# Kernel tuning notes

Hardware: AMD Instinct MI355X
Metric: run time of the kernel (lower is better)

The kernel has to match this reference:

```python
import jax, jax.numpy as jnp
import numpy as np

N = 40000        # nodes (shared across categories)
E = 600000       # edges per category graph
H = 2            # heads
C = 64           # hidden (out_channels per head)
IN_DIMS = [128, 128, 64]
FUSED = H * C * len(IN_DIMS)  # 384


def setup_inputs() -> dict:
    key = jax.random.key(0)
    ks = iter(jax.random.split(key, 64))
    d = {}
    for i, din in enumerate(IN_DIMS):
        d[f"x{i}"] = jax.random.normal(next(ks), (N, din), jnp.float32)
        d[f"ei{i}"] = jax.random.randint(next(ks), (2, E), 0, N)
        d[f"W{i}"] = jax.random.normal(next(ks), (din, H * C), jnp.float32) / np.sqrt(din)
        d[f"att_s{i}"] = jax.random.normal(next(ks), (H, C), jnp.float32) * 0.1
        d[f"att_d{i}"] = jax.random.normal(next(ks), (H, C), jnp.float32) * 0.1
        d[f"bias{i}"] = jnp.zeros((H * C,), jnp.float32)
    d["Wc1"] = jax.random.normal(next(ks), (FUSED, 128), jnp.float32) / np.sqrt(FUSED)
    d["bc1"] = jnp.zeros((128,), jnp.float32)
    d["Wc2"] = jax.random.normal(next(ks), (128, 1), jnp.float32) / np.sqrt(128.0)
    d["bc2"] = jnp.zeros((1,), jnp.float32)
    return d


def gat_conv(x, edge_index, W, att_s, att_d, bias):
    """PyG GATConv (concat=True, add_self_loops=True, eval mode)."""
    n = x.shape[0]
    xw = (x @ W).reshape(n, H, C)                       # [N,H,C]
    a_src = jnp.einsum('nhc,hc->nh', xw, att_s)         # [N,H]
    a_dst = jnp.einsum('nhc,hc->nh', xw, att_d)         # [N,H]
    loop = jnp.arange(n)
    src = jnp.concatenate([edge_index[0], loop])        # [E+N]
    dst = jnp.concatenate([edge_index[1], loop])
    e = jax.nn.leaky_relu(a_src[src] + a_dst[dst], 0.2)  # [E+N,H]
    # segment softmax over incoming edges per destination node
    m = jax.lax.stop_gradient(jax.ops.segment_max(e, dst, num_segments=n))
    ex = jnp.exp(e - m[dst])
    s = jax.ops.segment_sum(ex, dst, num_segments=n)
    alpha = ex / s[dst]                                  # [E+N,H]
    out = jax.ops.segment_sum(xw[src] * alpha[..., None], dst, num_segments=n)
    return out.reshape(n, H * C) + bias


def reference(x0, ei0, W0, att_s0, att_d0, bias0,
              x1, ei1, W1, att_s1, att_d1, bias1,
              x2, ei2, W2, att_s2, att_d2, bias2,
              Wc1, bc1, Wc2, bc2):
    h0 = jax.nn.elu(gat_conv(x0, ei0, W0, att_s0, att_d0, bias0))
    h1 = jax.nn.elu(gat_conv(x1, ei1, W1, att_s1, att_d1, bias1))
    h2 = jax.nn.elu(gat_conv(x2, ei2, W2, att_s2, att_d2, bias2))
    Hcat = jnp.concatenate([h0, h1, h2], axis=-1)        # [N, FUSED]
    hid = jax.nn.relu(Hcat @ Wc1 + bc1)
    return hid @ Wc2 + bc2                               # [N, 1]
```

## Files before the change

kernel.cpp:

```cpp
#include <hip/hip_runtime.h>
#include <cstdint>
#include <cstddef>


__device__ __forceinline__ float lrelu02(float x) { return x > 0.f ? x : 0.2f * x; }
__device__ __forceinline__ float elu1(float x) { return x > 0.f ? x : (__expf(x) - 1.f); }

__device__ __forceinline__ unsigned bfrne(float x) {
  unsigned u = __float_as_uint(x);
  return (u + 0x7FFFu + ((u >> 16) & 1u)) >> 16;
}
__device__ __forceinline__ unsigned pack2bf(float lo, float hi) {
  return bfrne(lo) | (bfrne(hi) << 16);
}
__device__ __forceinline__ float bflo2f(unsigned u) { return __uint_as_float(u << 16); }
__device__ __forceinline__ float bfhi2f(unsigned u) { return __uint_as_float(u & 0xFFFF0000u); }

typedef __attribute__((ext_vector_type(8))) short short8;
typedef __attribute__((ext_vector_type(4))) float f32x4;

#define SLICES 8
#define CAPX 448
#define BCAP (SLICES * CAPX)

#define SBS 512
#define SEPT 16
#define STB (SBS * SEPT)
#define NBINS_PAD 1024

__global__ void zeroB(int* __restrict__ a, int n) {
  int i = blockIdx.x * blockDim.x + threadIdx.x;
  if (i < n) a[i] = 0;
}

__global__ void w_swz(const float* __restrict__ W,
                      unsigned short* __restrict__ wsw, int nt) {
  int idx = blockIdx.x * blockDim.x + threadIdx.x;
  if (idx >= nt * 8 * 64) return;
  int l = idx & 63;
  int n = (idx >> 6) & 7;
  int t = idx >> 9;
  int col = n * 16 + (l & 15);
  int kbase = t * 32 + (l >> 4) * 8;
  uint4 o;
  o.x = pack2bf(W[(kbase + 0) * 128 + col], W[(kbase + 1) * 128 + col]);
  o.y = pack2bf(W[(kbase + 2) * 128 + col], W[(kbase + 3) * 128 + col]);
  o.z = pack2bf(W[(kbase + 4) * 128 + col], W[(kbase + 5) * 128 + col]);
  o.w = pack2bf(W[(kbase + 6) * 128 + col], W[(kbase + 7) * 128 + col]);
  *(uint4*)(wsw + (size_t)idx * 8) = o;
}

__global__ __launch_bounds__(256) void gemm_att_mfma(
    const float* __restrict__ X, const unsigned short* __restrict__ wsw,
    const float* __restrict__ att_s, const float* __restrict__ att_d,
    unsigned short* __restrict__ XWH, float* __restrict__ a_src,
    float* __restrict__ a_dst, int M, int K) {
  const int tid = threadIdx.x;
  const int l = tid & 63;
  const int w = tid >> 6;
  const int lrow = l & 15;
  const int lk = (l >> 4) * 8;
  const int row0 = blockIdx.x * 64 + w * 16;
  int arow = row0 + lrow; if (arow >= M) arow = M - 1;
  const float* aptr = X + (size_t)arow * K + lk;
  const unsigned short* bptr = wsw + (size_t)l * 8;
  const int nt = K >> 5;

  f32x4 acc[8];
#pragma unroll
  for (int n = 0; n < 8; ++n) acc[n] = (f32x4){0.f, 0.f, 0.f, 0.f};

  for (int t = 0; t < nt; ++t) {
    float4 xa = *(const float4*)(aptr + t * 32);
    float4 xb = *(const float4*)(aptr + t * 32 + 4);
    uint4 av;
    av.x = pack2bf(xa.x, xa.y);
    av.y = pack2bf(xa.z, xa.w);
    av.z = pack2bf(xb.x, xb.y);
    av.w = pack2bf(xb.z, xb.w);
    short8 af = __builtin_bit_cast(short8, av);
#pragma unroll
    for (int n = 0; n < 8; ++n) {
      uint4 bv = *(const uint4*)(bptr + (size_t)(t * 8 + n) * 512);
      short8 bf = __builtin_bit_cast(short8, bv);
      acc[n] = __builtin_amdgcn_mfma_f32_16x16x32_bf16(af, bf, acc[n], 0, 0, 0);
    }
  }

  float as_[8], ad_[8];
#pragma unroll
  for (int n = 0; n < 8; ++n) {
    int col = n * 16 + lrow;
    as_[n] = att_s[col];
    ad_[n] = att_d[col];
  }
#pragma unroll
  for (int r = 0; r < 4; ++r) {
    int wrow = row0 + (l >> 4) * 4 + r;
    const bool ok = wrow < M;
    float ps0 = 0.f, ps1 = 0.f, pd0 = 0.f, pd1 = 0.f;
#pragma unroll
    for (int n = 0; n < 8; ++n) {
      float v = acc[n][r];
      if (ok) XWH[(size_t)wrow * 128 + n * 16 + lrow] = (unsigned short)bfrne(v);
      if (n < 4) { ps0 = fmaf(v, as_[n], ps0); pd0 = fmaf(v, ad_[n], pd0); }
      else       { ps1 = fmaf(v, as_[n], ps1); pd1 = fmaf(v, ad_[n], pd1); }
    }
#pragma unroll
    for (int off = 1; off < 16; off <<= 1) {
      ps0 += __shfl_xor(ps0, off); ps1 += __shfl_xor(ps1, off);
      pd0 += __shfl_xor(pd0, off); pd1 += __shfl_xor(pd1, off);
    }
    if (lrow == 0 && ok) {
      ((float2*)a_src)[wrow] = make_float2(ps0, ps1);
      ((float2*)a_dst)[wrow] = make_float2(pd0, pd1);
    }
  }
}

__global__ __launch_bounds__(512) void scatter_p(
    const int* __restrict__ ei0, const int* __restrict__ ei1,
    const int* __restrict__ ei2, int E0, int E1, int E2,
    int nbpc, int* __restrict__ bktCnt, int* __restrict__ bkt) {
  __shared__ int hist[NBINS_PAD];
  __shared__ int binStart[NBINS_PAD];
  __shared__ int binResv[NBINS_PAD];
  __shared__ int fillB[NBINS_PAD];
  __shared__ int scanBuf[SBS];
  __shared__ int stage[STB];
  __shared__ int gdst[STB];
  const int tid = threadIdx.x;
  const int slice = blockIdx.x & (SLICES - 1);
  const int nbins = 3 * nbpc;
  const int c1 = E0, c2 = E0 + E1, totE = c2 + E2;
  const int eb = blockIdx.x * STB;

  for (int b = tid; b < NBINS_PAD; b += SBS) hist[b] = 0;
  __syncthreads();

  int binv[SEPT], payv[SEPT];
#pragma unroll
  for (int k = 0; k < SEPT; ++k) {
    int g = eb + k * SBS + tid;
    int bn = -1, pay = 0;
    if (g < totE) {
      int s, d, cat;
      if (g < c1)      { s = ei0[g]; d = ei0[E0 + g]; cat = 0; }
      else if (g < c2) { int t = g - c1; s = ei1[t]; d = ei1[E1 + t]; cat = 1; }
      else             { int t = g - c2; s = ei2[t]; d = ei2[E2 + t]; cat = 2; }
      bn = cat * nbpc + (d >> 7);
      pay = ((d & 127) << 16) | s;
      atomicAdd(&hist[bn], 1);
    }
    binv[k] = bn; payv[k] = pay;
  }
  __syncthreads();

  const int a0 = hist[tid * 2], a1 = hist[tid * 2 + 1];
  scanBuf[tid] = a0 + a1;
  __syncthreads();
  for (int off = 1; off < SBS; off <<= 1) {
    int v = (tid >= off) ? scanBuf[tid - off] : 0;
    __syncthreads();
    scanBuf[tid] += v;
    __syncthreads();
  }
  const int total = scanBuf[SBS - 1];
  const int base = (tid > 0) ? scanBuf[tid - 1] : 0;
  binStart[tid * 2] = base;
  binStart[tid * 2 + 1] = base + a0;

  for (int b = tid; b < NBINS_PAD; b += SBS) {
    fillB[b] = 0;
    int c = hist[b];
    if (c > 0 && b < nbins)
      binResv[b] = atomicAdd(&bktCnt[(b * SLICES + slice) * 16], c);
  }
  __syncthreads();

#pragma unroll
  for (int k = 0; k < SEPT; ++k) {
    int bn = binv[k];
    if (bn >= 0) {
      int f = atomicAdd(&fillB[bn], 1);
      int p = binStart[bn] + f;
      int go = binResv[bn] + f;
      stage[p] = payv[k];
      gdst[p] = (go < CAPX) ? ((bn * SLICES + slice) * CAPX + go) : -1;
    }
  }
  __syncthreads();

  for (int i = tid; i < total; i += SBS) {
    int g = gdst[i];
    if (g >= 0) bkt[g] = stage[i];
  }
}

__global__ __launch_bounds__(256) void sortbkt(
    int* __restrict__ bkt, const int* __restrict__ bktCnt,
    int2* __restrict__ offcnt, int Nn, int nbpc) {
  __shared__ int cntA[128], scanA[128], fillA[128];
  __shared__ int esort[BCAP];
  const int tid = threadIdx.x;
  const int b = blockIdx.x;
  const int cat = b / nbpc, bl = b - cat * nbpc, dBase = bl << 7;
  if (tid < 128) {
    cntA[tid] = (dBase + tid < Nn) ? 1 : 0;
    fillA[tid] = 0;
  }
  __syncthreads();
  int ns[SLICES];
#pragma unroll
  for (int s = 0; s < SLICES; ++s)
    ns[s] = min(bktCnt[(b * SLICES + s) * 16], CAPX);
#pragma unroll
  for (int s = 0; s < SLICES; ++s) {
    const int* seg = bkt + (size_t)(b * SLICES + s) * CAPX;
    for (int i = tid; i < ns[s]; i += 256) atomicAdd(&cntA[seg[i] >> 16], 1);
  }
  __syncthreads();
  if (tid < 128) scanA[tid] = cntA[tid];
  __syncthreads();
  for (int off = 1; off < 128; off <<= 1) {
    int t = (tid < 128 && tid >= off) ? scanA[tid - off] : 0;
    __syncthreads();
    if (tid < 128) scanA[tid] += t;
    __syncthreads();
  }
#pragma unroll
  for (int s = 0; s < SLICES; ++s) {
    const int* seg = bkt + (size_t)(b * SLICES + s) * CAPX;
    for (int i = tid; i < ns[s]; i += 256) {
      int v = seg[i];
      int n = v >> 16;
      int p = scanA[n] - cntA[n] + atomicAdd(&fillA[n], 1);
      esort[p] = v & 0xFFFF;
    }
  }
  if (tid < 128 && dBase + tid < Nn) esort[scanA[tid] - 1] = dBase + tid;
  __syncthreads();
  const int tot = scanA[127];
  int* outp = bkt + (size_t)b * BCAP;
  for (int i = tid; i < tot; i += 256) outp[i] = esort[i];
  if (tid < 128 && dBase + tid < Nn)
    offcnt[(size_t)cat * Nn + dBase + tid] =
        make_int2(b * BCAP + scanA[tid] - cntA[tid], cntA[tid]);
}

__global__ __launch_bounds__(256) void aggregate(
    const unsigned short* __restrict__ xwh, const float* __restrict__ a_src,
    const float* __restrict__ a_dst, const int2* __restrict__ offcnt,
    const int* __restrict__ adjS, const float* __restrict__ bias,
    unsigned short* __restrict__ ahc, int Nn) {
  const int node = (int)((blockIdx.x * (size_t)blockDim.x + threadIdx.x) >> 6);
  const int lane = threadIdx.x & 63;
  if (node >= Nn) return;
  const int2 oc = offcnt[node];
  const int base = oc.x, end = oc.x + oc.y;
  const float2 ad = ((const float2*)a_dst)[node];

  float m0 = -1e30f, s0 = 0.f, m1 = -1e30f, s1 = 0.f;
  int sv0 = 0; float ex0 = -1e30f, ey0 = -1e30f;
  for (int cb = base; cb < end; cb += 64) {
    int j = cb + lane;
    int sv = 0; float ex = -1e30f, ey = -1e30f;
    if (j < end) {
      sv = adjS[j];
      float2 as = ((const float2*)a_src)[sv];
      ex = lrelu02(as.x + ad.x);
      ey = lrelu02(as.y + ad.y);
      float nm0 = fmaxf(m0, ex);
      s0 = s0 * __expf(m0 - nm0) + __expf(ex - nm0); m0 = nm0;
      float nm1 = fmaxf(m1, ey);
      s1 = s1 * __expf(m1 - nm1) + __expf(ey - nm1); m1 = nm1;
    }
    if (cb == base) { sv0 = sv; ex0 = ex; ey0 = ey; }
  }
#pragma unroll
  for (int off = 32; off; off >>= 1) {
    float om0 = __shfl_xor(m0, off), os0 = __shfl_xor(s0, off);
    float nm0 = fmaxf(m0, om0);
    s0 = s0 * __expf(m0 - nm0) + os0 * __expf(om0 - nm0); m0 = nm0;
    float om1 = __shfl_xor(m1, off), os1 = __shfl_xor(s1, off);
    float nm1 = fmaxf(m1, om1);
    s1 = s1 * __expf(m1 - nm1) + os1 * __expf(om1 - nm1); m1 = nm1;
  }
  const float inv0 = 1.f / s0, inv1 = 1.f / s1;
  const bool h0 = (lane < 32);

  float2 acc = {0.f, 0.f};
  for (int cb = base; cb < end; cb += 64) {
    const int cnt = min(64, end - cb);
    int srcv; float w0v, w1v;
    if (cb == base) {
      srcv = sv0;
      w0v = __expf(ex0 - m0) * inv0;
      w1v = __expf(ey0 - m1) * inv1;
    } else {
      srcv = 0; float ex = -1e30f, ey = -1e30f;
      if (lane < cnt) {
        srcv = adjS[cb + lane];
        float2 as = ((const float2*)a_src)[srcv];
        ex = lrelu02(as.x + ad.x);
        ey = lrelu02(as.y + ad.y);
      }
      w0v = __expf(ex - m0) * inv0;
      w1v = __expf(ey - m1) * inv1;
    }
    int k = 0;
    for (; k + 4 <= cnt; k += 4) {
      int sa = __shfl(srcv, k),     sb = __shfl(srcv, k + 1);
      int sc = __shfl(srcv, k + 2), sd = __shfl(srcv, k + 3);
      unsigned ua = ((const unsigned*)(xwh + (size_t)sa * 128))[lane];
      unsigned ub = ((const unsigned*)(xwh + (size_t)sb * 128))[lane];
      unsigned uc = ((const unsigned*)(xwh + (size_t)sc * 128))[lane];
      unsigned ud = ((const unsigned*)(xwh + (size_t)sd * 128))[lane];
      float w0a = __shfl(w0v, k),     w1a = __shfl(w1v, k);
      float w0b = __shfl(w0v, k + 1), w1b = __shfl(w1v, k + 1);
      float w0c = __shfl(w0v, k + 2), w1c = __shfl(w1v, k + 2);
      float w0d = __shfl(w0v, k + 3), w1d = __shfl(w1v, k + 3);
      float wa = h0 ? w0a : w1a;
      float wb = h0 ? w0b : w1b;
      float wc = h0 ? w0c : w1c;
      float wd = h0 ? w0d : w1d;
      acc.x = fmaf(wa, bflo2f(ua), acc.x); acc.y = fmaf(wa, bfhi2f(ua), acc.y);
      acc.x = fmaf(wb, bflo2f(ub), acc.x); acc.y = fmaf(wb, bfhi2f(ub), acc.y);
      acc.x = fmaf(wc, bflo2f(uc), acc.x); acc.y = fmaf(wc, bfhi2f(uc), acc.y);
      acc.x = fmaf(wd, bflo2f(ud), acc.x); acc.y = fmaf(wd, bfhi2f(ud), acc.y);
    }
    for (; k < cnt; ++k) {
      int s = __shfl(srcv, k);
      float w0b_ = __shfl(w0v, k), w1b_ = __shfl(w1v, k);
      float w = h0 ? w0b_ : w1b_;
      unsigned u = ((const unsigned*)(xwh + (size_t)s * 128))[lane];
      acc.x = fmaf(w, bflo2f(u), acc.x);
      acc.y = fmaf(w, bfhi2f(u), acc.y);
    }
  }
  const float2 bv = ((const float2*)bias)[lane];
  ((unsigned*)(ahc + (size_t)node * 384))[lane] =
      pack2bf(elu1(acc.x + bv.x), elu1(acc.y + bv.y));
}

__global__ __launch_bounds__(256) void final_mlp_mfma(
    const unsigned short* __restrict__ ah, const unsigned short* __restrict__ wsw,
    const float* __restrict__ bc1, const float* __restrict__ Wc2,
    const float* __restrict__ bc2, float* __restrict__ out, int Nn) {
  const int tid = threadIdx.x;
  const int l = tid & 63;
  const int w = tid >> 6;
  const int lrow = l & 15;
  const int lk = (l >> 4) * 8;
  int row = blockIdx.x * 64 + w * 16 + lrow;
  int arow = row < Nn ? row : Nn - 1;
  const unsigned short* aptr = ah + (size_t)arow * 384 + lk;
  const unsigned short* bptr = wsw + (size_t)l * 8;

  f32x4 acc[8];
#pragma unroll
  for (int n = 0; n < 8; ++n) acc[n] = (f32x4){0.f, 0.f, 0.f, 0.f};

  for (int t = 0; t < 12; ++t) {
    uint4 av = *(const uint4*)(aptr + t * 32);
    short8 af = __builtin_bit_cast(short8, av);
#pragma unroll
    for (int n = 0; n < 8; ++n) {
      uint4 bv = *(const uint4*)(bptr + (size_t)(t * 8 + n) * 512);
      short8 bf = __builtin_bit_cast(short8, bv);
      acc[n] = __builtin_amdgcn_mfma_f32_16x16x32_bf16(af, bf, acc[n], 0, 0, 0);
    }
  }

  float bcv[8], w2v[8];
#pragma unroll
  for (int n = 0; n < 8; ++n) {
    int col = n * 16 + lrow;
    bcv[n] = bc1[col];
    w2v[n] = Wc2[col];
  }
  float p[4];
#pragma unroll
  for (int r = 0; r < 4; ++r) {
    float s = 0.f;
#pragma unroll
    for (int n = 0; n < 8; ++n)
      s = fmaf(fmaxf(acc[n][r] + bcv[n], 0.f), w2v[n], s);
#pragma unroll
    for (int off = 1; off < 16; off <<= 1) s += __shfl_xor(s, off);
    p[r] = s;
  }
  if (lrow == 0) {
    int orow = blockIdx.x * 64 + w * 16 + (l >> 4) * 4;
    float b2 = bc2[0];
    if (orow + 3 < Nn) {
      float4 o = {p[0] + b2, p[1] + b2, p[2] + b2, p[3] + b2};
      *(float4*)(out + orow) = o;
    } else {
#pragma unroll
      for (int r = 0; r < 4; ++r)
        if (orow + r < Nn) out[orow + r] = p[r] + b2;
    }
  }
}

extern "C" void kernel_launch(void* const* d_in, const int* in_sizes, int n_in,
                              void* d_out, int out_size, void* d_ws, size_t ws_size,
                              hipStream_t stream) {
  const int Nn = out_size;
  const int E0 = in_sizes[1] / 2;
  const int E1 = in_sizes[7] / 2;
  const int E2 = in_sizes[13] / 2;
  const int totE = E0 + E1 + E2;
  const int Nt = 3 * Nn;
  const int nbpc = (Nn + 127) / 128;
  const int NB = 3 * nbpc;

  char* base = (char*)d_ws;
  size_t off = 0;
  auto carve = [&](size_t bytes) -> void* {
    off = (off + 255) & ~(size_t)255;
    void* p = base + off;
    off += bytes;
    return p;
  };
  unsigned short* xwh = (unsigned short*)carve((size_t)Nn * 128 * 2);
  unsigned short* ah  = (unsigned short*)carve((size_t)Nn * 384 * 2);
  unsigned short* wsw = (unsigned short*)carve((size_t)12 * 8 * 64 * 8 * 2);
  unsigned short* wswx = (unsigned short*)carve((size_t)3 * 4 * 8 * 64 * 8 * 2);
  float* a_src3 = (float*)carve((size_t)Nt * 2 * 4);
  float* a_dst3 = (float*)carve((size_t)Nt * 2 * 4);
  int*  bktCnt  = (int*)carve((size_t)NB * SLICES * 16 * 4);
  int2* offcnt3 = (int2*)carve((size_t)Nt * 8);
  int*  bkt     = (int*)carve((size_t)NB * BCAP * 4);
  (void)ws_size; (void)n_in;

  const int* ei0 = (const int*)d_in[1];
  const int* ei1 = (const int*)d_in[7];
  const int* ei2 = (const int*)d_in[13];

  const int ncnt = NB * SLICES * 16;
  zeroB<<<(ncnt + 255) / 256, 256, 0, stream>>>(bktCnt, ncnt);
  w_swz<<<(12 * 8 * 64 + 255) / 256, 256, 0, stream>>>(
      (const float*)d_in[18], wsw, 12);
  for (int cat = 0; cat < 3; ++cat) {
    const int K = in_sizes[6 * cat] / Nn;
    w_swz<<<((K >> 5) * 8 * 64 + 255) / 256, 256, 0, stream>>>(
        (const float*)d_in[6 * cat + 2], wswx + (size_t)cat * 4 * 8 * 64 * 8,
        K >> 5);
  }
  scatter_p<<<(totE + STB - 1) / STB, SBS, 0, stream>>>(
      ei0, ei1, ei2, E0, E1, E2, nbpc, bktCnt, bkt);
  sortbkt<<<NB, 256, 0, stream>>>(bkt, bktCnt, offcnt3, Nn, nbpc);

  for (int cat = 0; cat < 3; ++cat) {
    const float* x   = (const float*)d_in[6 * cat + 0];
    const float* ats = (const float*)d_in[6 * cat + 3];
    const float* atd = (const float*)d_in[6 * cat + 4];
    const float* bia = (const float*)d_in[6 * cat + 5];
    const int K = in_sizes[6 * cat] / Nn;
    float* a_src_c = a_src3 + (size_t)cat * Nn * 2;
    float* a_dst_c = a_dst3 + (size_t)cat * Nn * 2;

    gemm_att_mfma<<<(Nn + 63) / 64, 256, 0, stream>>>(
        x, wswx + (size_t)cat * 4 * 8 * 64 * 8, ats, atd, xwh,
        a_src_c, a_dst_c, Nn, K);
    aggregate<<<((size_t)Nn * 64 + 255) / 256, 256, 0, stream>>>(
        xwh, a_src_c, a_dst_c, offcnt3 + (size_t)cat * Nn, bkt, bia,
        ah + (size_t)cat * 128, Nn);
  }

  final_mlp_mfma<<<(Nn + 63) / 64, 256, 0, stream>>>(
      ah, wsw, (const float*)d_in[19], (const float*)d_in[20],
      (const float*)d_in[21], (float*)d_out, Nn);
}
```

Before: 323.5 us.

## Aggregate four nodes per wavefront with 16-lane groups and 16-byte gathers

The GAT aggregation kernel now gives each destination node a 16-lane group instead of a full 64-lane wavefront, so one wave handles four nodes. Each lane loads 8 bf16 features with a uint4 gather and keeps 8 accumulators. Edge weights for both heads travel between lanes packed as fp16 pairs. This is meant to cut idle lanes for low-degree nodes (about 16 edges on average) and to issue fewer, wider memory transactions, at the cost of divergence across the four nodes, since the loop runs to the wave-wide maximum degree, and of fp16 rounding on the attention weights.

Result: faster. 296.6 us (-8.3%).

```diff
diff --git a/kernel.cpp b/kernel.cpp
--- a/kernel.cpp
+++ b/kernel.cpp
@@ -1,4 +1,5 @@
 #include <hip/hip_runtime.h>
+#include <hip/hip_fp16.h>
 #include <cstdint>
 #include <cstddef>
 
@@ -15,6 +16,17 @@
 }
 __device__ __forceinline__ float bflo2f(unsigned u) { return __uint_as_float(u << 16); }
 __device__ __forceinline__ float bfhi2f(unsigned u) { return __uint_as_float(u & 0xFFFF0000u); }
+
+__device__ __forceinline__ unsigned pack2half(float lo, float hi) {
+  __half2 h2 = __floats2half2_rn(lo, hi);
+  return __builtin_bit_cast(unsigned, h2);
+}
+__device__ __forceinline__ float h2lo(unsigned u) {
+  return __half2float(__low2half(__builtin_bit_cast(__half2, u)));
+}
+__device__ __forceinline__ float h2hi(unsigned u) {
+  return __half2float(__high2half(__builtin_bit_cast(__half2, u)));
+}
 
 typedef __attribute__((ext_vector_type(8))) short short8;
 typedef __attribute__((ext_vector_type(4))) float f32x4;
@@ -253,20 +265,25 @@
     const float* __restrict__ a_dst, const int2* __restrict__ offcnt,
     const int* __restrict__ adjS, const float* __restrict__ bias,
     unsigned short* __restrict__ ahc, int Nn) {
-  const int node = (int)((blockIdx.x * (size_t)blockDim.x + threadIdx.x) >> 6);
-  const int lane = threadIdx.x & 63;
-  if (node >= Nn) return;
-  const int2 oc = offcnt[node];
-  const int base = oc.x, end = oc.x + oc.y;
-  const float2 ad = ((const float2*)a_dst)[node];
+  const int tid = threadIdx.x;
+  const int lane = tid & 63;
+  const int li = lane & 15;
+  const int gb = lane & 48;
+  const int wid = (int)((blockIdx.x * (size_t)blockDim.x + tid) >> 6);
+  const int node = wid * 4 + (lane >> 4);
+  const bool nok = node < Nn;
+  const int cnode = nok ? node : Nn - 1;
+  const int2 oc = offcnt[cnode];
+  const int base = oc.x;
+  const int cnt = oc.y;
+  const float2 ad = ((const float2*)a_dst)[cnode];
 
   float m0 = -1e30f, s0 = 0.f, m1 = -1e30f, s1 = 0.f;
   int sv0 = 0; float ex0 = -1e30f, ey0 = -1e30f;
-  for (int cb = base; cb < end; cb += 64) {
-    int j = cb + lane;
+  for (int cb = 0; cb < cnt; cb += 16) {
     int sv = 0; float ex = -1e30f, ey = -1e30f;
-    if (j < end) {
-      sv = adjS[j];
+    if (cb + li < cnt) {
+      sv = adjS[base + cb + li];
       float2 as = ((const float2*)a_src)[sv];
       ex = lrelu02(as.x + ad.x);
       ey = lrelu02(as.y + ad.y);
@@ -275,10 +292,10 @@
       float nm1 = fmaxf(m1, ey);
       s1 = s1 * __expf(m1 - nm1) + __expf(ey - nm1); m1 = nm1;
     }
-    if (cb == base) { sv0 = sv; ex0 = ex; ey0 = ey; }
-  }
-#pragma unroll
-  for (int off = 32; off; off >>= 1) {
+    if (cb == 0) { sv0 = sv; ex0 = ex; ey0 = ey; }
+  }
+#pragma unroll
+  for (int off = 8; off; off >>= 1) {
     float om0 = __shfl_xor(m0, off), os0 = __shfl_xor(s0, off);
     float nm0 = fmaxf(m0, om0);
     s0 = s0 * __expf(m0 - nm0) + os0 * __expf(om0 - nm0); m0 = nm0;
@@ -287,60 +304,77 @@
     s1 = s1 * __expf(m1 - nm1) + os1 * __expf(om1 - nm1); m1 = nm1;
   }
   const float inv0 = 1.f / s0, inv1 = 1.f / s1;
-  const bool h0 = (lane < 32);
-
-  float2 acc = {0.f, 0.f};
-  for (int cb = base; cb < end; cb += 64) {
-    const int cnt = min(64, end - cb);
-    int srcv; float w0v, w1v;
-    if (cb == base) {
-      srcv = sv0;
-      w0v = __expf(ex0 - m0) * inv0;
-      w1v = __expf(ey0 - m1) * inv1;
-    } else {
-      srcv = 0; float ex = -1e30f, ey = -1e30f;
-      if (lane < cnt) {
-        srcv = adjS[cb + lane];
-        float2 as = ((const float2*)a_src)[srcv];
+
+  int mc = cnt;
+  mc = max(mc, __shfl_xor(mc, 16));
+  mc = max(mc, __shfl_xor(mc, 32));
+
+  const bool hlo = (li < 8);
+  float acc[8];
+#pragma unroll
+  for (int c = 0; c < 8; ++c) acc[c] = 0.f;
+
+  for (int cb = 0; cb < mc; cb += 16) {
+    int sv; float ex, ey;
+    if (cb == 0) { sv = sv0; ex = ex0; ey = ey0; }
+    else {
+      sv = 0; ex = -1e30f; ey = -1e30f;
+      if (cb + li < cnt) {
+        sv = adjS[base + cb + li];
+        float2 as = ((const float2*)a_src)[sv];
         ex = lrelu02(as.x + ad.x);
         ey = lrelu02(as.y + ad.y);
       }
-      w0v = __expf(ex - m0) * inv0;
-      w1v = __expf(ey - m1) * inv1;
-    }
+    }
+    const float w0 = __expf(ex - m0) * inv0;
+    const float w1 = __expf(ey - m1) * inv1;
+    const unsigned wpk = pack2half(w0, w1);
+
+    int cc = cnt - cb; cc = cc < 0 ? 0 : (cc > 16 ? 16 : cc);
+    cc = max(cc, __shfl_xor(cc, 16));
+    cc = max(cc, __shfl_xor(cc, 32));
+
     int k = 0;
-    for (; k + 4 <= cnt; k += 4) {
-      int sa = __shfl(srcv, k),     sb = __shfl(srcv, k + 1);
-      int sc = __shfl(srcv, k + 2), sd = __shfl(srcv, k + 3);
-      unsigned ua = ((const unsigned*)(xwh + (size_t)sa * 128))[lane];
-      unsigned ub = ((const unsigned*)(xwh + (size_t)sb * 128))[lane];
-      unsigned uc = ((const unsigned*)(xwh + (size_t)sc * 128))[lane];
-      unsigned ud = ((const unsigned*)(xwh + (size_t)sd * 128))[lane];
-      float w0a = __shfl(w0v, k),     w1a = __shfl(w1v, k);
-      float w0b = __shfl(w0v, k + 1), w1b = __shfl(w1v, k + 1);
-      float w0c = __shfl(w0v, k + 2), w1c = __shfl(w1v, k + 2);
-      float w0d = __shfl(w0v, k + 3), w1d = __shfl(w1v, k + 3);
-      float wa = h0 ? w0a : w1a;
-      float wb = h0 ? w0b : w1b;
-      float wc = h0 ? w0c : w1c;
-      float wd = h0 ? w0d : w1d;
-      acc.x = fmaf(wa, bflo2f(ua), acc.x); acc.y = fmaf(wa, bfhi2f(ua), acc.y);
-      acc.x = fmaf(wb, bflo2f(ub), acc.x); acc.y = fmaf(wb, bfhi2f(ub), acc.y);
-      acc.x = fmaf(wc, bflo2f(uc), acc.x); acc.y = fmaf(wc, bfhi2f(uc), acc.y);
-      acc.x = fmaf(wd, bflo2f(ud), acc.x); acc.y = fmaf(wd, bfhi2f(ud), acc.y);
-    }
-    for (; k < cnt; ++k) {
-      int s = __shfl(srcv, k);
-      float w0b_ = __shfl(w0v, k), w1b_ = __shfl(w1v, k);
-      float w = h0 ? w0b_ : w1b_;
-      unsigned u = ((const unsigned*)(xwh + (size_t)s * 128))[lane];
-      acc.x = fmaf(w, bflo2f(u), acc.x);
-      acc.y = fmaf(w, bfhi2f(u), acc.y);
-    }
-  }
-  const float2 bv = ((const float2*)bias)[lane];
-  ((unsigned*)(ahc + (size_t)node * 384))[lane] =
-      pack2bf(elu1(acc.x + bv.x), elu1(acc.y + bv.y));
+    for (; k + 2 <= cc; k += 2) {
+      int ska = __shfl(sv, gb + k);
+      int skb = __shfl(sv, gb + k + 1);
+      unsigned wka = __shfl(wpk, gb + k);
+      unsigned wkb = __shfl(wpk, gb + k + 1);
+      uint4 ua = *(const uint4*)(xwh + (size_t)ska * 128 + li * 8);
+      uint4 ub = *(const uint4*)(xwh + (size_t)skb * 128 + li * 8);
+      float wa = hlo ? h2lo(wka) : h2hi(wka);
+      float wb = hlo ? h2lo(wkb) : h2hi(wkb);
+      acc[0] = fmaf(wa, bflo2f(ua.x), acc[0]); acc[1] = fmaf(wa, bfhi2f(ua.x), acc[1]);
+      acc[2] = fmaf(wa, bflo2f(ua.y), acc[2]); acc[3] = fmaf(wa, bfhi2f(ua.y), acc[3]);
+      acc[4] = fmaf(wa, bflo2f(ua.z), acc[4]); acc[5] = fmaf(wa, bfhi2f(ua.z), acc[5]);
+      acc[6] = fmaf(wa, bflo2f(ua.w), acc[6]); acc[7] = fmaf(wa, bfhi2f(ua.w), acc[7]);
+      acc[0] = fmaf(wb, bflo2f(ub.x), acc[0]); acc[1] = fmaf(wb, bfhi2f(ub.x), acc[1]);
+      acc[2] = fmaf(wb, bflo2f(ub.y), acc[2]); acc[3] = fmaf(wb, bfhi2f(ub.y), acc[3]);
+      acc[4] = fmaf(wb, bflo2f(ub.z), acc[4]); acc[5] = fmaf(wb, bfhi2f(ub.z), acc[5]);
+      acc[6] = fmaf(wb, bflo2f(ub.w), acc[6]); acc[7] = fmaf(wb, bfhi2f(ub.w), acc[7]);
+    }
+    for (; k < cc; ++k) {
+      int sk = __shfl(sv, gb + k);
+      unsigned wk = __shfl(wpk, gb + k);
+      float w = hlo ? h2lo(wk) : h2hi(wk);
+      uint4 u = *(const uint4*)(xwh + (size_t)sk * 128 + li * 8);
+      acc[0] = fmaf(w, bflo2f(u.x), acc[0]); acc[1] = fmaf(w, bfhi2f(u.x), acc[1]);
+      acc[2] = fmaf(w, bflo2f(u.y), acc[2]); acc[3] = fmaf(w, bfhi2f(u.y), acc[3]);
+      acc[4] = fmaf(w, bflo2f(u.z), acc[4]); acc[5] = fmaf(w, bfhi2f(u.z), acc[5]);
+      acc[6] = fmaf(w, bflo2f(u.w), acc[6]); acc[7] = fmaf(w, bfhi2f(u.w), acc[7]);
+    }
+  }
+
+  if (nok) {
+    const float4 b0 = *(const float4*)(bias + li * 8);
+    const float4 b1 = *(const float4*)(bias + li * 8 + 4);
+    uint4 o;
+    o.x = pack2bf(elu1(acc[0] + b0.x), elu1(acc[1] + b0.y));
+    o.y = pack2bf(elu1(acc[2] + b0.z), elu1(acc[3] + b0.w));
+    o.z = pack2bf(elu1(acc[4] + b1.x), elu1(acc[5] + b1.y));
+    o.w = pack2bf(elu1(acc[6] + b1.z), elu1(acc[7] + b1.w));
+    *(uint4*)(ahc + (size_t)node * 384 + li * 8) = o;
+  }
 }
 
 __global__ __launch_bounds__(256) void final_mlp_mfma(
@@ -465,7 +499,7 @@
     gemm_att_mfma<<<(Nn + 63) / 64, 256, 0, stream>>>(
         x, wswx + (size_t)cat * 4 * 8 * 64 * 8, ats, atd, xwh,
         a_src_c, a_dst_c, Nn, K);
-    aggregate<<<((size_t)Nn * 64 + 255) / 256, 256, 0, stream>>>(
+    aggregate<<<(Nn + 15) / 16, 256, 0, stream>>>(
         xwh, a_src_c, a_dst_c, offcnt3 + (size_t)cat * Nn, bkt, bia,
         ah + (size_t)cat * 128, Nn);
   }
```
